# Optimization experiments

Hardware: AMD Instinct MI355X
Metric: run time of the kernel (lower is better)

## Reference

```python
import jax, jax.numpy as jnp
import numpy as np

N_NODES = 50000
N_EDGES = 800000
D_IN = 64
D_OUT = 64


def setup_inputs() -> dict:
    key = jax.random.key(0)
    k1, k2, k3, k4, k5 = jax.random.split(key, 5)
    feat = jax.random.normal(k1, (N_NODES, D_IN), dtype=jnp.float32)
    # torch Linear layout: W [out_feats, in_feats]
    W = jax.random.normal(k2, (D_OUT, D_IN), dtype=jnp.float32) * (1.0 / np.sqrt(D_IN))
    b = jax.random.normal(k3, (D_OUT,), dtype=jnp.float32) * 0.01
    eps = jnp.zeros((1,), dtype=jnp.float32)
    src = jax.random.randint(k4, (N_EDGES,), 0, N_NODES, dtype=jnp.int32)
    dst = jax.random.randint(k5, (N_EDGES,), 0, N_NODES, dtype=jnp.int32)
    return {"feat": feat, "W": W, "b": b, "eps": eps, "src": src, "dst": dst}


def reference(feat, W, b, eps, src, dst):
    # message = feat[src]; sum-aggregate per destination node
    neigh = jax.ops.segment_sum(feat[src], dst, num_segments=N_NODES)  # [N, D_in]
    rst = (1.0 + eps) * feat + neigh                                   # eps-scaled residual
    out = rst @ W.T + b                                                # Linear (torch layout)
    return out
```

## Files before the change

### kernel.cpp

```cpp
#include <hip/hip_runtime.h>

constexpr int N_NODES = 50000;
constexpr int N_EDGES = 800000;
constexpr int D = 64;

constexpr int NREG = 256;
constexpr int RSZ = 196;
constexpr int EPB = 3136;
constexpr int NBINB = 256;
constexpr int CELLCAP = 64;
constexpr int RECAP = 4608;

constexpr int MT = 13;

constexpr int WS_CNT2 = 0;
constexpr int WS_RBUF = NREG * NBINB;
constexpr size_t WS_HB_BYTE = (size_t)(WS_RBUF + (size_t)NREG * NBINB * CELLCAP) * 4;

typedef __attribute__((ext_vector_type(8))) short short8v;
typedef __attribute__((ext_vector_type(4))) float f32x4;

__device__ __forceinline__ ushort to_bf16(float x) {
  unsigned u = __float_as_uint(x);
  u += 0x7FFF + ((u >> 16) & 1);
  return (ushort)(u >> 16);
}
__device__ __forceinline__ float bf_lo(unsigned u) {
  return __uint_as_float(u << 16);
}
__device__ __forceinline__ float bf_hi(unsigned u) {
  return __uint_as_float(u & 0xFFFF0000u);
}
__device__ __forceinline__ float bf_val(ushort h) {
  return __uint_as_float(((unsigned)h) << 16);
}

__global__ __launch_bounds__(1024) void prep_kernel(
    const float4* __restrict__ feat4, const int* __restrict__ src,
    const int* __restrict__ dst, ushort* __restrict__ hb,
    int* __restrict__ cnt2, unsigned* __restrict__ rbuf) {
  __shared__ int cur[NREG];
  __shared__ unsigned scell[NREG * CELLCAP];
  int tid = threadIdx.x, blk = blockIdx.x;
  if (tid < NREG) cur[tid] = 0;

  int e0 = blk * EPB + tid * 4;
  bool valid = (tid * 4 < EPB) && (e0 + 4 <= N_EDGES);
  int4 d4 = {0, 0, 0, 0}, s4 = {0, 0, 0, 0};
  if (valid) {
    d4 = *reinterpret_cast<const int4*>(dst + e0);
    s4 = *reinterpret_cast<const int4*>(src + e0);
  }

  for (int t = blk * 1024 + tid; t < N_NODES * D / 4; t += NBINB * 1024) {
    float4 f = feat4[t];
    ushort4 h;
    h.x = to_bf16(f.x); h.y = to_bf16(f.y);
    h.z = to_bf16(f.z); h.w = to_bf16(f.w);
    *reinterpret_cast<ushort4*>(hb + t * 4) = h;
  }
  __syncthreads();

  if (valid) {
    const int dd[4] = {d4.x, d4.y, d4.z, d4.w};
    const int ss[4] = {s4.x, s4.y, s4.z, s4.w};
#pragma unroll
    for (int k = 0; k < 4; ++k) {
      int r = dd[k] / RSZ;
      unsigned pk = ((unsigned)(dd[k] - r * RSZ) << 16) | (unsigned)ss[k];
      int p = atomicAdd(&cur[r], 1);
      if (p < CELLCAP) scell[r * CELLCAP + p] = pk;
    }
  }
  __syncthreads();

  {
    int cell = tid >> 2, sub = tid & 3;
    int c = cur[cell];
    if (c > CELLCAP) c = CELLCAP;
    unsigned* gp = rbuf + (size_t)(cell * NBINB + blk) * CELLCAP;
    const unsigned* sp = scell + cell * CELLCAP;
    for (int i = sub * 4; i < c; i += 16)
      *reinterpret_cast<uint4*>(gp + i) = *reinterpret_cast<const uint4*>(sp + i);
  }
  if (tid < NREG) {
    int c = cur[tid];
    cnt2[tid * NBINB + blk] = (c > CELLCAP) ? CELLCAP : c;
  }
}

__global__ __launch_bounds__(1024) void gin_kernel(
    const float* __restrict__ feat, const ushort* __restrict__ hb,
    const float* __restrict__ W, const float* __restrict__ b,
    const float* __restrict__ eps, const int* __restrict__ cnt2,
    const unsigned* __restrict__ rbuf, float* __restrict__ out) {
  __shared__ __align__(16) char pool[MT * 16 * 72 * 2];
  unsigned* ebuf = reinterpret_cast<unsigned*>(pool);
  ushort* rstH = reinterpret_cast<ushort*>(pool);
  __shared__ ushort sorted[RECAP];
  __shared__ ushort WbH[8 * 64 * 8];
  __shared__ ushort WbL[8 * 64 * 8];
  __shared__ float b_lds[D];
  __shared__ int cellstart[NBINB + 1];
  __shared__ int hist[RSZ], nstart[RSZ + 1], cursor[RSZ];
  __shared__ int wsum[4], wsum2[4];
  __shared__ int wq;

  int tid = threadIdx.x, r = blockIdx.x;
  int lane = tid & 63, wv = tid >> 6;

  if (tid < 512) {
    int tile = tid >> 6, l = tid & 63;
    int tk = tile >> 2, tn = tile & 3;
    int n = tn * 16 + (l & 15);
    int kb = tk * 32 + ((l >> 4) << 3);
    const float4 w0 = *reinterpret_cast<const float4*>(W + (n << 6) + kb);
    const float4 w1 = *reinterpret_cast<const float4*>(W + (n << 6) + kb + 4);
    float wf[8] = {w0.x, w0.y, w0.z, w0.w, w1.x, w1.y, w1.z, w1.w};
    ushort hh[8], ll[8];
#pragma unroll
    for (int e = 0; e < 8; ++e) {
      ushort h = to_bf16(wf[e]);
      hh[e] = h;
      ll[e] = to_bf16(wf[e] - bf_val(h));
    }
    uint4 vH, vL;
    vH.x = hh[0] | ((unsigned)hh[1] << 16); vH.y = hh[2] | ((unsigned)hh[3] << 16);
    vH.z = hh[4] | ((unsigned)hh[5] << 16); vH.w = hh[6] | ((unsigned)hh[7] << 16);
    vL.x = ll[0] | ((unsigned)ll[1] << 16); vL.y = ll[2] | ((unsigned)ll[3] << 16);
    vL.z = ll[4] | ((unsigned)ll[5] << 16); vL.w = ll[6] | ((unsigned)ll[7] << 16);
    *reinterpret_cast<uint4*>(&WbH[(tile * 64 + l) * 8]) = vH;
    *reinterpret_cast<uint4*>(&WbL[(tile * 64 + l) * 8]) = vL;
  }
  if (tid < D) b_lds[tid] = b[tid];
  if (tid < RSZ) hist[tid] = 0;
  if (tid == 0) wq = 0;

  int c = (tid < NBINB) ? cnt2[r * NBINB + tid] : 0;
  int inc = c;
#pragma unroll
  for (int dlt = 1; dlt < 64; dlt <<= 1) {
    int t = __shfl_up(inc, (unsigned)dlt, 64);
    if (lane >= dlt) inc += t;
  }
  if (tid < 256 && lane == 63) wsum[wv] = inc;
  __syncthreads();
  if (tid < 256) {
    int prefix = inc - c;
    if (wv > 0) prefix += wsum[0];
    if (wv > 1) prefix += wsum[1];
    if (wv > 2) prefix += wsum[2];
    if (tid < NBINB) cellstart[tid] = prefix;
  }
  if (tid == 0) cellstart[NBINB] = wsum[0] + wsum[1] + wsum[2] + wsum[3];
  __syncthreads();
  int T = cellstart[NBINB];
  if (T > RECAP) T = RECAP;

  {
    int cell = tid >> 2, sub = tid & 3;
    if (cell < NBINB) {
      int cs = cellstart[cell];
      int cc = cellstart[cell + 1] - cs;
      const unsigned* cp = rbuf + (size_t)(r * NBINB + cell) * CELLCAP;
      for (int i = sub * 4; i < cc; i += 16) {
        uint4 v = *reinterpret_cast<const uint4*>(cp + i);
        if (cs + i + 0 < T && i + 0 < cc) ebuf[cs + i + 0] = v.x;
        if (cs + i + 1 < T && i + 1 < cc) ebuf[cs + i + 1] = v.y;
        if (cs + i + 2 < T && i + 2 < cc) ebuf[cs + i + 2] = v.z;
        if (cs + i + 3 < T && i + 3 < cc) ebuf[cs + i + 3] = v.w;
      }
    }
  }
  __syncthreads();

  for (int e = tid; e < T; e += 1024) atomicAdd(&hist[ebuf[e] >> 16], 1);
  __syncthreads();

  int h = (tid < RSZ) ? hist[tid] : 0;
  int inc2 = h;
#pragma unroll
  for (int dlt = 1; dlt < 64; dlt <<= 1) {
    int t = __shfl_up(inc2, (unsigned)dlt, 64);
    if (lane >= dlt) inc2 += t;
  }
  if (tid < 256 && lane == 63) wsum2[wv] = inc2;
  __syncthreads();
  if (tid < 256) {
    int prefix = inc2 - h;
    if (wv > 0) prefix += wsum2[0];
    if (wv > 1) prefix += wsum2[1];
    if (wv > 2) prefix += wsum2[2];
    if (tid < RSZ) {
      nstart[tid] = prefix;
      cursor[tid] = prefix;
    }
  }
  if (tid == 0) nstart[RSZ] = wsum2[0] + wsum2[1] + wsum2[2] + wsum2[3];
  __syncthreads();
  for (int e = tid; e < T; e += 1024) {
    unsigned pk = ebuf[e];
    int p = atomicAdd(&cursor[pk >> 16], 1);
    sorted[p] = (ushort)(pk & 0xFFFFu);
  }
  __syncthreads();

  int j8 = (tid & 7) << 3;
  float s = 1.0f + eps[0];

  for (;;) {
    int n = 0;
    if ((tid & 7) == 0) n = atomicAdd(&wq, 1);
    n = __shfl(n, 0, 8);
    if (n >= RSZ) break;

    int node = r * RSZ + n;
    if (node >= N_NODES) continue;

    float acc[8];
    {
      const float4 fa = *reinterpret_cast<const float4*>(feat + (node << 6) + j8);
      const float4 fb = *reinterpret_cast<const float4*>(feat + (node << 6) + j8 + 4);
      acc[0] = s * fa.x; acc[1] = s * fa.y; acc[2] = s * fa.z; acc[3] = s * fa.w;
      acc[4] = s * fb.x; acc[5] = s * fb.y; acc[6] = s * fb.z; acc[7] = s * fb.w;
    }

    int e = nstart[n], e1 = nstart[n + 1];
    for (; e + 8 <= e1; e += 8) {
      int i0 = sorted[e + 0], i1 = sorted[e + 1], i2 = sorted[e + 2], i3 = sorted[e + 3];
      int i4_ = sorted[e + 4], i5 = sorted[e + 5], i6 = sorted[e + 6], i7 = sorted[e + 7];
      const uint4 h0 = *reinterpret_cast<const uint4*>(hb + (i0 << 6) + j8);
      const uint4 h1 = *reinterpret_cast<const uint4*>(hb + (i1 << 6) + j8);
      const uint4 h2 = *reinterpret_cast<const uint4*>(hb + (i2 << 6) + j8);
      const uint4 h3 = *reinterpret_cast<const uint4*>(hb + (i3 << 6) + j8);
      const uint4 h4 = *reinterpret_cast<const uint4*>(hb + (i4_ << 6) + j8);
      const uint4 h5 = *reinterpret_cast<const uint4*>(hb + (i5 << 6) + j8);
      const uint4 h6 = *reinterpret_cast<const uint4*>(hb + (i6 << 6) + j8);
      const uint4 h7 = *reinterpret_cast<const uint4*>(hb + (i7 << 6) + j8);
      acc[0] += (bf_lo(h0.x) + bf_lo(h1.x)) + (bf_lo(h2.x) + bf_lo(h3.x))
              + (bf_lo(h4.x) + bf_lo(h5.x)) + (bf_lo(h6.x) + bf_lo(h7.x));
      acc[1] += (bf_hi(h0.x) + bf_hi(h1.x)) + (bf_hi(h2.x) + bf_hi(h3.x))
              + (bf_hi(h4.x) + bf_hi(h5.x)) + (bf_hi(h6.x) + bf_hi(h7.x));
      acc[2] += (bf_lo(h0.y) + bf_lo(h1.y)) + (bf_lo(h2.y) + bf_lo(h3.y))
              + (bf_lo(h4.y) + bf_lo(h5.y)) + (bf_lo(h6.y) + bf_lo(h7.y));
      acc[3] += (bf_hi(h0.y) + bf_hi(h1.y)) + (bf_hi(h2.y) + bf_hi(h3.y))
              + (bf_hi(h4.y) + bf_hi(h5.y)) + (bf_hi(h6.y) + bf_hi(h7.y));
      acc[4] += (bf_lo(h0.z) + bf_lo(h1.z)) + (bf_lo(h2.z) + bf_lo(h3.z))
              + (bf_lo(h4.z) + bf_lo(h5.z)) + (bf_lo(h6.z) + bf_lo(h7.z));
      acc[5] += (bf_hi(h0.z) + bf_hi(h1.z)) + (bf_hi(h2.z) + bf_hi(h3.z))
              + (bf_hi(h4.z) + bf_hi(h5.z)) + (bf_hi(h6.z) + bf_hi(h7.z));
      acc[6] += (bf_lo(h0.w) + bf_lo(h1.w)) + (bf_lo(h2.w) + bf_lo(h3.w))
              + (bf_lo(h4.w) + bf_lo(h5.w)) + (bf_lo(h6.w) + bf_lo(h7.w));
      acc[7] += (bf_hi(h0.w) + bf_hi(h1.w)) + (bf_hi(h2.w) + bf_hi(h3.w))
              + (bf_hi(h4.w) + bf_hi(h5.w)) + (bf_hi(h6.w) + bf_hi(h7.w));
    }
    for (; e < e1; ++e) {
      int sn = sorted[e];
      const uint4 hv = *reinterpret_cast<const uint4*>(hb + (sn << 6) + j8);
      acc[0] += bf_lo(hv.x); acc[1] += bf_hi(hv.x);
      acc[2] += bf_lo(hv.y); acc[3] += bf_hi(hv.y);
      acc[4] += bf_lo(hv.z); acc[5] += bf_hi(hv.z);
      acc[6] += bf_lo(hv.w); acc[7] += bf_hi(hv.w);
    }

    unsigned p0 = (unsigned)to_bf16(acc[0]) | ((unsigned)to_bf16(acc[1]) << 16);
    unsigned p1 = (unsigned)to_bf16(acc[2]) | ((unsigned)to_bf16(acc[3]) << 16);
    unsigned p2 = (unsigned)to_bf16(acc[4]) | ((unsigned)to_bf16(acc[5]) << 16);
    unsigned p3 = (unsigned)to_bf16(acc[6]) | ((unsigned)to_bf16(acc[7]) << 16);
    uint4 vv; vv.x = p0; vv.y = p1; vv.z = p2; vv.w = p3;
    *reinterpret_cast<uint4*>(&rstH[n * 72 + j8]) = vv;
  }
  __syncthreads();

  {
    int l = tid & 63;
    int lr = l & 15, lc = l >> 4;
    for (int t = wv; t < MT * 4; t += 16) {
      int mt = t >> 2, nt = t & 3;
      int m0 = mt << 4, n0 = nt << 4;
      float bc = b_lds[n0 + lr];
      f32x4 cacc = {bc, bc, bc, bc};
#pragma unroll
      for (int tk = 0; tk < 2; ++tk) {
        short8v a = *reinterpret_cast<const short8v*>(&rstH[(m0 + lr) * 72 + tk * 32 + lc * 8]);
        short8v wh = *reinterpret_cast<const short8v*>(&WbH[((tk * 4 + nt) * 64 + l) * 8]);
        short8v wl = *reinterpret_cast<const short8v*>(&WbL[((tk * 4 + nt) * 64 + l) * 8]);
        cacc = __builtin_amdgcn_mfma_f32_16x16x32_bf16(a, wh, cacc, 0, 0, 0);
        cacc = __builtin_amdgcn_mfma_f32_16x16x32_bf16(a, wl, cacc, 0, 0, 0);
      }
#pragma unroll
      for (int rr = 0; rr < 4; ++rr) {
        int row = m0 + lc * 4 + rr;
        int node = r * RSZ + row;
        if (row < RSZ && node < N_NODES)
          out[(node << 6) + n0 + lr] = cacc[rr];
      }
    }
  }
}

extern "C" void kernel_launch(void* const* d_in, const int* in_sizes, int n_in,
                              void* d_out, int out_size, void* d_ws, size_t ws_size,
                              hipStream_t stream) {
  const float* feat = (const float*)d_in[0];
  const float* W    = (const float*)d_in[1];
  const float* b    = (const float*)d_in[2];
  const float* eps  = (const float*)d_in[3];
  const int*   src  = (const int*)d_in[4];
  const int*   dst  = (const int*)d_in[5];
  float* out = (float*)d_out;

  int* ws = (int*)d_ws;
  int* cnt2      = ws + WS_CNT2;
  unsigned* rbuf = (unsigned*)(ws + WS_RBUF);
  ushort* hb     = (ushort*)((char*)d_ws + WS_HB_BYTE);

  hipLaunchKernelGGL(prep_kernel, dim3(NBINB), dim3(1024), 0, stream,
                     (const float4*)feat, src, dst, hb, cnt2, rbuf);
  hipLaunchKernelGGL(gin_kernel, dim3(NREG), dim3(1024), 0, stream,
                     feat, hb, W, b, eps, cnt2, rbuf, out);
}
```

Baseline: 102.3 us.

## Fuse prep and aggregation kernels into one cooperative launch with grid sync

Merges the binning/bf16-conversion kernel and the aggregation+linear kernel into one cooperative kernel separated by a grid-wide barrier. Shared memory is manually pooled and reused across the two phases. Per-cell capacity drops from 64 to 48, with a padded LDS stride to ease bank conflicts. This saves a kernel launch and the gap between launches, but adds a grid-sync cost and a higher risk of dropping edges when a cell overflows the smaller capacity.

```diff
diff --git a/kernel.cpp b/kernel.cpp
--- a/kernel.cpp
+++ b/kernel.cpp
@@ -1,4 +1,5 @@
 #include <hip/hip_runtime.h>
+#include <hip/hip_cooperative_groups.h>
 
 constexpr int N_NODES = 50000;
 constexpr int N_EDGES = 800000;
@@ -8,9 +9,9 @@
 constexpr int RSZ = 196;
 constexpr int EPB = 3136;
 constexpr int NBINB = 256;
-constexpr int CELLCAP = 64;
+constexpr int CELLCAP = 48;
+constexpr int SCSTR = 52;
 constexpr int RECAP = 4608;
-
 constexpr int MT = 13;
 
 constexpr int WS_CNT2 = 0;
@@ -35,79 +36,85 @@
   return __uint_as_float(((unsigned)h) << 16);
 }
 
-__global__ __launch_bounds__(1024) void prep_kernel(
-    const float4* __restrict__ feat4, const int* __restrict__ src,
-    const int* __restrict__ dst, ushort* __restrict__ hb,
-    int* __restrict__ cnt2, unsigned* __restrict__ rbuf) {
-  __shared__ int cur[NREG];
-  __shared__ unsigned scell[NREG * CELLCAP];
+__global__ __launch_bounds__(1024) void fused_kernel(
+    const float* __restrict__ feat, const int* __restrict__ src,
+    const int* __restrict__ dst, const float* __restrict__ W,
+    const float* __restrict__ b, const float* __restrict__ eps,
+    int* __restrict__ cnt2, unsigned* __restrict__ rbuf,
+    ushort* __restrict__ hb, float* __restrict__ out) {
+  __shared__ __align__(16) char smem[61440];
   int tid = threadIdx.x, blk = blockIdx.x;
-  if (tid < NREG) cur[tid] = 0;
-
-  int e0 = blk * EPB + tid * 4;
-  bool valid = (tid * 4 < EPB) && (e0 + 4 <= N_EDGES);
-  int4 d4 = {0, 0, 0, 0}, s4 = {0, 0, 0, 0};
-  if (valid) {
-    d4 = *reinterpret_cast<const int4*>(dst + e0);
-    s4 = *reinterpret_cast<const int4*>(src + e0);
-  }
-
-  for (int t = blk * 1024 + tid; t < N_NODES * D / 4; t += NBINB * 1024) {
-    float4 f = feat4[t];
-    ushort4 h;
-    h.x = to_bf16(f.x); h.y = to_bf16(f.y);
-    h.z = to_bf16(f.z); h.w = to_bf16(f.w);
-    *reinterpret_cast<ushort4*>(hb + t * 4) = h;
-  }
-  __syncthreads();
-
-  if (valid) {
-    const int dd[4] = {d4.x, d4.y, d4.z, d4.w};
-    const int ss[4] = {s4.x, s4.y, s4.z, s4.w};
-#pragma unroll
-    for (int k = 0; k < 4; ++k) {
-      int r = dd[k] / RSZ;
-      unsigned pk = ((unsigned)(dd[k] - r * RSZ) << 16) | (unsigned)ss[k];
-      int p = atomicAdd(&cur[r], 1);
-      if (p < CELLCAP) scell[r * CELLCAP + p] = pk;
-    }
-  }
-  __syncthreads();
 
   {
-    int cell = tid >> 2, sub = tid & 3;
-    int c = cur[cell];
-    if (c > CELLCAP) c = CELLCAP;
-    unsigned* gp = rbuf + (size_t)(cell * NBINB + blk) * CELLCAP;
-    const unsigned* sp = scell + cell * CELLCAP;
-    for (int i = sub * 4; i < c; i += 16)
-      *reinterpret_cast<uint4*>(gp + i) = *reinterpret_cast<const uint4*>(sp + i);
-  }
-  if (tid < NREG) {
-    int c = cur[tid];
-    cnt2[tid * NBINB + blk] = (c > CELLCAP) ? CELLCAP : c;
-  }
-}
-
-__global__ __launch_bounds__(1024) void gin_kernel(
-    const float* __restrict__ feat, const ushort* __restrict__ hb,
-    const float* __restrict__ W, const float* __restrict__ b,
-    const float* __restrict__ eps, const int* __restrict__ cnt2,
-    const unsigned* __restrict__ rbuf, float* __restrict__ out) {
-  __shared__ __align__(16) char pool[MT * 16 * 72 * 2];
-  unsigned* ebuf = reinterpret_cast<unsigned*>(pool);
-  ushort* rstH = reinterpret_cast<ushort*>(pool);
-  __shared__ ushort sorted[RECAP];
-  __shared__ ushort WbH[8 * 64 * 8];
-  __shared__ ushort WbL[8 * 64 * 8];
-  __shared__ float b_lds[D];
-  __shared__ int cellstart[NBINB + 1];
-  __shared__ int hist[RSZ], nstart[RSZ + 1], cursor[RSZ];
-  __shared__ int wsum[4], wsum2[4];
-  __shared__ int wq;
-
-  int tid = threadIdx.x, r = blockIdx.x;
+    int* cur = reinterpret_cast<int*>(smem);
+    unsigned* scell = reinterpret_cast<unsigned*>(smem) + 256;
+    if (tid < NREG) cur[tid] = 0;
+
+    const float4* feat4 = reinterpret_cast<const float4*>(feat);
+    int e0 = blk * EPB + tid * 4;
+    bool valid = (tid * 4 < EPB) && (e0 + 4 <= N_EDGES);
+    int4 d4 = {0, 0, 0, 0}, s4 = {0, 0, 0, 0};
+    if (valid) {
+      d4 = *reinterpret_cast<const int4*>(dst + e0);
+      s4 = *reinterpret_cast<const int4*>(src + e0);
+    }
+
+    for (int t = blk * 1024 + tid; t < N_NODES * D / 4; t += NBINB * 1024) {
+      float4 f = feat4[t];
+      ushort4 h;
+      h.x = to_bf16(f.x); h.y = to_bf16(f.y);
+      h.z = to_bf16(f.z); h.w = to_bf16(f.w);
+      *reinterpret_cast<ushort4*>(hb + t * 4) = h;
+    }
+    __syncthreads();
+
+    if (valid) {
+      const int dd[4] = {d4.x, d4.y, d4.z, d4.w};
+      const int ss[4] = {s4.x, s4.y, s4.z, s4.w};
+#pragma unroll
+      for (int k = 0; k < 4; ++k) {
+        int r = dd[k] / RSZ;
+        unsigned pk = ((unsigned)(dd[k] - r * RSZ) << 16) | (unsigned)ss[k];
+        int p = atomicAdd(&cur[r], 1);
+        if (p < CELLCAP) scell[r * SCSTR + p] = pk;
+      }
+    }
+    __syncthreads();
+
+    {
+      int cell = tid >> 2, sub = tid & 3;
+      int c = cur[cell];
+      if (c > CELLCAP) c = CELLCAP;
+      unsigned* gp = rbuf + (size_t)(cell * NBINB + blk) * CELLCAP;
+      const unsigned* sp = scell + cell * SCSTR;
+      for (int i = sub * 4; i < c; i += 16)
+        *reinterpret_cast<uint4*>(gp + i) = *reinterpret_cast<const uint4*>(sp + i);
+    }
+    if (tid < NREG) {
+      int c = cur[tid];
+      cnt2[tid * NBINB + blk] = (c > CELLCAP) ? CELLCAP : c;
+    }
+  }
+
+  __threadfence();
+  cooperative_groups::this_grid().sync();
+
+  int r = blk;
   int lane = tid & 63, wv = tid >> 6;
+
+  unsigned* ebuf = reinterpret_cast<unsigned*>(smem);
+  ushort* rstH = reinterpret_cast<ushort*>(smem);
+  ushort* sorted = reinterpret_cast<ushort*>(smem + 29952);
+  ushort* WbH = reinterpret_cast<ushort*>(smem + 39168);
+  ushort* WbL = reinterpret_cast<ushort*>(smem + 47360);
+  float* b_lds = reinterpret_cast<float*>(smem + 55552);
+  int* cellstart = reinterpret_cast<int*>(smem + 55808);
+  int* hist = reinterpret_cast<int*>(smem + 56848);
+  int* nstart = reinterpret_cast<int*>(smem + 57632);
+  int* cursor = reinterpret_cast<int*>(smem + 58432);
+  int* wsum = reinterpret_cast<int*>(smem + 59216);
+  int* wsum2 = reinterpret_cast<int*>(smem + 59232);
+  int* wq = reinterpret_cast<int*>(smem + 59248);
 
   if (tid < 512) {
     int tile = tid >> 6, l = tid & 63;
@@ -134,7 +141,7 @@
   }
   if (tid < D) b_lds[tid] = b[tid];
   if (tid < RSZ) hist[tid] = 0;
-  if (tid == 0) wq = 0;
+  if (tid == 0) *wq = 0;
 
   int c = (tid < NBINB) ? cnt2[r * NBINB + tid] : 0;
   int inc = c;
@@ -210,7 +217,7 @@
 
   for (;;) {
     int n = 0;
-    if ((tid & 7) == 0) n = atomicAdd(&wq, 1);
+    if ((tid & 7) == 0) n = atomicAdd(wq, 1);
     n = __shfl(n, 0, 8);
     if (n >= RSZ) break;
 
@@ -315,8 +322,9 @@
   unsigned* rbuf = (unsigned*)(ws + WS_RBUF);
   ushort* hb     = (ushort*)((char*)d_ws + WS_HB_BYTE);
 
-  hipLaunchKernelGGL(prep_kernel, dim3(NBINB), dim3(1024), 0, stream,
-                     (const float4*)feat, src, dst, hb, cnt2, rbuf);
-  hipLaunchKernelGGL(gin_kernel, dim3(NREG), dim3(1024), 0, stream,
-                     feat, hb, W, b, eps, cnt2, rbuf, out);
-}
+  void* args[] = {(void*)&feat, (void*)&src, (void*)&dst, (void*)&W,
+                  (void*)&b,    (void*)&eps, (void*)&cnt2, (void*)&rbuf,
+                  (void*)&hb,   (void*)&out};
+  hipLaunchCooperativeKernel((const void*)fused_kernel, dim3(NREG), dim3(1024),
+                             args, 0, stream);
+}
```

After: 231.3 us. 2.26x slower.
